# Performance work log

Hardware: AMD Instinct MI355X
Metric: run time of the kernel (lower is better)

The kernel has to match this reference:

```python
import jax, jax.numpy as jnp
import numpy as np

TIMESTEPS = 1000


def setup_inputs() -> dict:
    key = jax.random.key(0)
    k1, k2 = jax.random.split(key)
    rec = jax.random.uniform(k1, (64, 1, 256, 256), dtype=jnp.float32)
    tgt = jax.random.uniform(k2, (64, 1, 256, 256), dtype=jnp.float32)
    return {"reconstructed_image": rec, "target_image": tgt}


def _holographic_transform(img):
    # img: [B, 1, H, W] -> out: [B, 1, H, TIMESTEPS]
    # Original: for every nonzero pixel (x, y) with value v, writes
    #   out[b, 0, x, int(v * timesteps) - 1] = y
    # iterating in row-major (y ascending) order, so for duplicate targets the
    B, C, H, W = img.shape
    x = img[:, 0]  # [B, H, W]
    q = (x * TIMESTEPS).astype(jnp.int32) - 1
    # torch negative indexing wraps (q = -1 -> timesteps - 1); zero pixels are
    # skipped, so route them to an out-of-range index and drop.
    q = jnp.where(x != 0, q % TIMESTEPS, TIMESTEPS)  # [B, H, W]
    y_vals = jnp.broadcast_to(jnp.arange(W, dtype=img.dtype), (B, H, W))
    b_idx = jnp.arange(B)[:, None, None]
    h_idx = jnp.arange(H)[None, :, None]
    out = jnp.zeros((B, 1, H, TIMESTEPS), dtype=img.dtype)
    out = out.at[b_idx, 0, h_idx, q].max(y_vals, mode="drop")
    return out


def reference(reconstructed_image, target_image):
    rec_holo = _holographic_transform(reconstructed_image)
    tgt_holo = _holographic_transform(target_image)
    return jnp.mean((rec_holo - tgt_holo) ** 2)
```

## Files before the change

### kernel.cpp

```cpp
#include <hip/hip_runtime.h>

#define TIMESTEPS 1000
#define NROWS 16384
#define ROWS_PER_WAVE 4
#define WAVES_PER_BLOCK 4
#define NBLOCKS (NROWS / (ROWS_PER_WAVE * WAVES_PER_BLOCK))
#define NPARTIALS (NROWS / ROWS_PER_WAVE)
#define TOTAL_ELEMS 16384000.0

__global__ __launch_bounds__(256) void holo_row_loss(
    const float* __restrict__ rec,
    const float* __restrict__ tgt,
    float* __restrict__ partials)
{
    __shared__ int bins[WAVES_PER_BLOCK][2048];

    const int tid  = threadIdx.x;
    const int wav  = tid >> 6;
    const int lane = tid & 63;
    const int gw   = blockIdx.x * WAVES_PER_BLOCK + wav;

    int* __restrict__ binw = &bins[wav][0];

    int4 z4; z4.x = 0; z4.y = 0; z4.z = 0; z4.w = 0;
    int4* zb = (int4*)binw;
#pragma unroll
    for (int j = 0; j < 8; ++j) zb[j * 64 + lane] = z4;
    __builtin_amdgcn_wave_barrier();

    const float4* rec4 = (const float4*)rec;
    const float4* tgt4 = (const float4*)tgt;

    float s = 0.0f;

#pragma unroll 1
    for (int r = 0; r < ROWS_PER_WAVE; ++r) {
        const int row = gw * ROWS_PER_WAVE + r;
        const float4 xr = rec4[row * 64 + lane];
        const float4 xt = tgt4[row * 64 + lane];

        int qr[4], qt[4];
#pragma unroll
        for (int j = 0; j < 4; ++j) {
            const float vr = (&xr.x)[j];
            const float vt = (&xt.x)[j];
            const int   w  = lane * 4 + j;
            int q = (int)(vr * 1000.0f) - 1;
            if (q < 0) q += TIMESTEPS;
            if (vr != 0.0f) { atomicMax(&binw[q], w); qr[j] = q; }
            else            { qr[j] = 1012; }
            q = (int)(vt * 1000.0f) - 1;
            if (q < 0) q += TIMESTEPS;
            if (vt != 0.0f) { atomicMax(&binw[1024 + q], w); qt[j] = q; }
            else            { qt[j] = 1012; }
        }
        __builtin_amdgcn_wave_barrier();

        const int4* r4 = (const int4*)binw;
        const int4* t4 = (const int4*)(binw + 1024);
#pragma unroll
        for (int k = 0; k < 4; ++k) {
            const int4 a = r4[k * 64 + lane];
            const int4 b = t4[k * 64 + lane];
            const float d0 = (float)(a.x - b.x);
            const float d1 = (float)(a.y - b.y);
            const float d2 = (float)(a.z - b.z);
            const float d3 = (float)(a.w - b.w);
            s = fmaf(d0, d0, s);
            s = fmaf(d1, d1, s);
            s = fmaf(d2, d2, s);
            s = fmaf(d3, d3, s);
        }
        __builtin_amdgcn_wave_barrier();

#pragma unroll
        for (int j = 0; j < 4; ++j) {
            binw[qr[j]] = 0;
            binw[1024 + qt[j]] = 0;
        }
        __builtin_amdgcn_wave_barrier();
    }

    for (int off = 32; off > 0; off >>= 1) s += __shfl_down(s, off, 64);
    if (lane == 0) partials[gw] = s;
}

__global__ __launch_bounds__(256) void reduce_partials(
    const float* __restrict__ partials,
    float* __restrict__ out)
{
    __shared__ double wave_sums[4];
    const int tid = threadIdx.x;
    double s = 0.0;
#pragma unroll
    for (int i = 0; i < NPARTIALS / 256; ++i)
        s += (double)partials[i * 256 + tid];
    for (int off = 32; off > 0; off >>= 1) s += __shfl_down(s, off, 64);
    if ((tid & 63) == 0) wave_sums[tid >> 6] = s;
    __syncthreads();
    if (tid == 0) {
        double tot = wave_sums[0] + wave_sums[1] + wave_sums[2] + wave_sums[3];
        out[0] = (float)(tot / TOTAL_ELEMS);
    }
}

extern "C" void kernel_launch(void* const* d_in, const int* in_sizes, int n_in,
                              void* d_out, int out_size, void* d_ws, size_t ws_size,
                              hipStream_t stream)
{
    const float* rec = (const float*)d_in[0];
    const float* tgt = (const float*)d_in[1];
    float* out = (float*)d_out;
    float* partials = (float*)d_ws;

    holo_row_loss<<<NBLOCKS, 256, 0, stream>>>(rec, tgt, partials);
    reduce_partials<<<1, 256, 0, stream>>>(partials, out);
}
```

Measured before the change: 75.76 us.

## Tag bins with row generation to skip clearing, prefetch rows, block-level reduction

Each atomicMax value is tagged with a per-row generation offset ((r+1)<<8), and readers subtract the base and clamp at zero. Stale entries from earlier rows are therefore ignored, which removes the per-row bin-clearing pass and its extra wave barrier. All four rows' inputs are loaded up front so the global loads overlap. The per-wave partials are also combined within each block into one double, which cuts the final reduction to 1024 entries. The cost is a few more registers and a block-wide __syncthreads at the end.

New measurement: 95.61 us. 26.2% more time.

```diff
diff --git a/kernel.cpp b/kernel.cpp
--- a/kernel.cpp
+++ b/kernel.cpp
@@ -5,15 +5,15 @@
 #define ROWS_PER_WAVE 4
 #define WAVES_PER_BLOCK 4
 #define NBLOCKS (NROWS / (ROWS_PER_WAVE * WAVES_PER_BLOCK))
-#define NPARTIALS (NROWS / ROWS_PER_WAVE)
 #define TOTAL_ELEMS 16384000.0
 
 __global__ __launch_bounds__(256) void holo_row_loss(
     const float* __restrict__ rec,
     const float* __restrict__ tgt,
-    float* __restrict__ partials)
+    double* __restrict__ block_partials)
 {
     __shared__ int bins[WAVES_PER_BLOCK][2048];
+    __shared__ float wave_sums[WAVES_PER_BLOCK];
 
     const int tid  = threadIdx.x;
     const int wav  = tid >> 6;
@@ -26,33 +26,35 @@
     int4* zb = (int4*)binw;
 #pragma unroll
     for (int j = 0; j < 8; ++j) zb[j * 64 + lane] = z4;
-    __builtin_amdgcn_wave_barrier();
 
     const float4* rec4 = (const float4*)rec;
     const float4* tgt4 = (const float4*)tgt;
+    float4 xr[ROWS_PER_WAVE], xt[ROWS_PER_WAVE];
+#pragma unroll
+    for (int r = 0; r < ROWS_PER_WAVE; ++r) {
+        const int row = gw * ROWS_PER_WAVE + r;
+        xr[r] = rec4[row * 64 + lane];
+        xt[r] = tgt4[row * 64 + lane];
+    }
+    __builtin_amdgcn_wave_barrier();
 
     float s = 0.0f;
 
 #pragma unroll 1
     for (int r = 0; r < ROWS_PER_WAVE; ++r) {
-        const int row = gw * ROWS_PER_WAVE + r;
-        const float4 xr = rec4[row * 64 + lane];
-        const float4 xt = tgt4[row * 64 + lane];
+        const int base = (r + 1) << 8;
 
-        int qr[4], qt[4];
 #pragma unroll
         for (int j = 0; j < 4; ++j) {
-            const float vr = (&xr.x)[j];
-            const float vt = (&xt.x)[j];
+            const float vr = (&xr[r].x)[j];
+            const float vt = (&xt[r].x)[j];
             const int   w  = lane * 4 + j;
             int q = (int)(vr * 1000.0f) - 1;
             if (q < 0) q += TIMESTEPS;
-            if (vr != 0.0f) { atomicMax(&binw[q], w); qr[j] = q; }
-            else            { qr[j] = 1012; }
+            if (vr != 0.0f) atomicMax(&binw[q], base | w);
             q = (int)(vt * 1000.0f) - 1;
             if (q < 0) q += TIMESTEPS;
-            if (vt != 0.0f) { atomicMax(&binw[1024 + q], w); qt[j] = q; }
-            else            { qt[j] = 1012; }
+            if (vt != 0.0f) atomicMax(&binw[1024 + q], base | w);
         }
         __builtin_amdgcn_wave_barrier();
 
@@ -62,39 +64,42 @@
         for (int k = 0; k < 4; ++k) {
             const int4 a = r4[k * 64 + lane];
             const int4 b = t4[k * 64 + lane];
-            const float d0 = (float)(a.x - b.x);
-            const float d1 = (float)(a.y - b.y);
-            const float d2 = (float)(a.z - b.z);
-            const float d3 = (float)(a.w - b.w);
+            const int wa0 = max(a.x - base, 0), wb0 = max(b.x - base, 0);
+            const int wa1 = max(a.y - base, 0), wb1 = max(b.y - base, 0);
+            const int wa2 = max(a.z - base, 0), wb2 = max(b.z - base, 0);
+            const int wa3 = max(a.w - base, 0), wb3 = max(b.w - base, 0);
+            const float d0 = (float)(wa0 - wb0);
+            const float d1 = (float)(wa1 - wb1);
+            const float d2 = (float)(wa2 - wb2);
+            const float d3 = (float)(wa3 - wb3);
             s = fmaf(d0, d0, s);
             s = fmaf(d1, d1, s);
             s = fmaf(d2, d2, s);
             s = fmaf(d3, d3, s);
         }
         __builtin_amdgcn_wave_barrier();
-
-#pragma unroll
-        for (int j = 0; j < 4; ++j) {
-            binw[qr[j]] = 0;
-            binw[1024 + qt[j]] = 0;
-        }
-        __builtin_amdgcn_wave_barrier();
     }
 
     for (int off = 32; off > 0; off >>= 1) s += __shfl_down(s, off, 64);
-    if (lane == 0) partials[gw] = s;
+    if (lane == 0) wave_sums[wav] = s;
+    __syncthreads();
+    if (tid == 0) {
+        double bsum = (double)wave_sums[0] + (double)wave_sums[1]
+                    + (double)wave_sums[2] + (double)wave_sums[3];
+        block_partials[blockIdx.x] = bsum;
+    }
 }
 
 __global__ __launch_bounds__(256) void reduce_partials(
-    const float* __restrict__ partials,
+    const double* __restrict__ block_partials,
     float* __restrict__ out)
 {
     __shared__ double wave_sums[4];
     const int tid = threadIdx.x;
     double s = 0.0;
 #pragma unroll
-    for (int i = 0; i < NPARTIALS / 256; ++i)
-        s += (double)partials[i * 256 + tid];
+    for (int i = 0; i < NBLOCKS / 256; ++i)
+        s += block_partials[i * 256 + tid];
     for (int off = 32; off > 0; off >>= 1) s += __shfl_down(s, off, 64);
     if ((tid & 63) == 0) wave_sums[tid >> 6] = s;
     __syncthreads();
@@ -111,8 +116,8 @@
     const float* rec = (const float*)d_in[0];
     const float* tgt = (const float*)d_in[1];
     float* out = (float*)d_out;
-    float* partials = (float*)d_ws;
+    double* block_partials = (double*)d_ws;
 
-    holo_row_loss<<<NBLOCKS, 256, 0, stream>>>(rec, tgt, partials);
-    reduce_partials<<<1, 256, 0, stream>>>(partials, out);
+    holo_row_loss<<<NBLOCKS, 256, 0, stream>>>(rec, tgt, block_partials);
+    reduce_partials<<<1, 256, 0, stream>>>(block_partials, out);
 }
```
